# Kernel optimization log

Hardware: AMD Instinct MI355X
Metric: run time of the kernel (lower is better)

## Reference

```python
import jax, jax.numpy as jnp
import numpy as np

BS, RAL, LAL = 128, 1024, 256
CS, VOC, HFS, EMB = 256, 34, 512, 256


def setup_inputs() -> dict:
    key0 = jax.random.key(0)
    ks = jax.random.split(key0, 16)
    s = 0.02
    # mask from random valid lengths (at least 1 valid frame per example)
    lengths = jax.random.randint(ks[15], (BS,), RAL // 2, RAL + 1)
    mask = (jnp.arange(RAL)[None, :] < lengths[:, None]).astype(jnp.float32)
    return {
        "key": jax.random.normal(ks[0], (BS, RAL, CS), jnp.float32),
        "val": jax.random.normal(ks[1], (BS, RAL, CS), jnp.float32),
        "mask": mask,
        "emb": jax.random.normal(ks[2], (VOC, EMB), jnp.float32) * s,
        "Wih_a": jax.random.normal(ks[3], (4 * HFS, EMB + CS), jnp.float32) * s,
        "Whh_a": jax.random.normal(ks[4], (4 * HFS, HFS), jnp.float32) * s,
        "bih_a": jnp.zeros((4 * HFS,), jnp.float32),
        "bhh_a": jnp.zeros((4 * HFS,), jnp.float32),
        "Wih_b": jax.random.normal(ks[5], (4 * HFS, HFS), jnp.float32) * s,
        "Whh_b": jax.random.normal(ks[6], (4 * HFS, HFS), jnp.float32) * s,
        "bih_b": jnp.zeros((4 * HFS,), jnp.float32),
        "bhh_b": jnp.zeros((4 * HFS,), jnp.float32),
        "Wq": jax.random.normal(ks[7], (CS, HFS), jnp.float32) * s,
        "bq": jnp.zeros((CS,), jnp.float32),
        "Wc": jax.random.normal(ks[8], (VOC, HFS + CS), jnp.float32) * s,
        "bc": jnp.zeros((VOC,), jnp.float32),
        "y": jax.random.randint(ks[9], (BS, LAL), 0, VOC, jnp.int32),
    }


def _lstm_cell(x, h, c, Wih, Whh, bih, bhh):
    z = x @ Wih.T + bih + h @ Whh.T + bhh  # (BS, 4H)
    i, f, g, o = jnp.split(z, 4, axis=-1)
    i, f, o = jax.nn.sigmoid(i), jax.nn.sigmoid(f), jax.nn.sigmoid(o)
    g = jnp.tanh(g)
    c2 = f * c + i * g
    return o * jnp.tanh(c2), c2


def _attend(key, val, query, mask):
    # energy: (BS, RAL) = bmm(key, query[...,None])
    energy = jnp.einsum("brc,bc->br", key, query)
    att = jax.nn.softmax(energy, axis=1) * mask
    att = att / jnp.sum(att, axis=1, keepdims=True)
    return jnp.einsum("br,brc->bc", att, val)  # context (BS, CS)


def reference(key, val, mask, emb, Wih_a, Whh_a, bih_a, bhh_a,
              Wih_b, Whh_b, bih_b, bhh_b, Wq, bq, Wc, bc, y):
    bs = y.shape[0]
    z = jnp.zeros((bs, HFS), jnp.float32)
    init = (z, z, z, z, jnp.zeros((bs, CS), jnp.float32))

    def step(carry, y_t):
        ha, ca, hb, cb, ctx = carry
        e = emb[y_t]  # (BS, EMB)
        x = jnp.concatenate([e, ctx], axis=1)
        ha, ca = _lstm_cell(x, ha, ca, Wih_a, Whh_a, bih_a, bhh_a)
        hb, cb = _lstm_cell(ha, hb, cb, Wih_b, Whh_b, bih_b, bhh_b)
        query = hb @ Wq.T + bq  # (BS, CS)
        ctx = _attend(key, val, query, mask)
        logits = jnp.concatenate([hb, ctx], axis=1) @ Wc.T + bc  # (BS, VOC)
        return (ha, ca, hb, cb, ctx), logits

    _, preds = jax.lax.scan(step, init, y.T)  # (LAL, BS, VOC)
    return jnp.transpose(preds, (1, 0, 2))  # (BS, LAL, VOC)
```

## Files before the change

kernel.cpp:

```cpp
#include <hip/hip_runtime.h>
#include <cstdint>
#include <cstddef>

static constexpr int BS  = 128;
static constexpr int RAL = 1024;
static constexpr int LAL = 256;
static constexpr int CS  = 256;
static constexpr int VOC = 34;
static constexpr int HFS = 512;
static constexpr int EMB = 256;

typedef float  f32x4  __attribute__((ext_vector_type(4)));
typedef short  bf16x8 __attribute__((ext_vector_type(8)));

static __device__ __forceinline__ float bflo(unsigned int u) {
    return __builtin_bit_cast(float, u << 16);
}
static __device__ __forceinline__ float bfhi(unsigned int u) {
    return __builtin_bit_cast(float, u & 0xffff0000u);
}
static __device__ __forceinline__ unsigned short f2bf(float f) {
    unsigned int x = __builtin_bit_cast(unsigned int, f);
    x = (x + 0x7fffu + ((x >> 16) & 1u)) >> 16;
    return (unsigned short)x;
}
static __device__ __forceinline__ float sigf(float x)   { return 1.0f / (1.0f + __expf(-x)); }
static __device__ __forceinline__ float tanhf_(float x) { return 1.0f - 2.0f / (__expf(2.0f * x) + 1.0f); }

__global__ void cvt4_kernel(const float4* __restrict__ in, ushort4* __restrict__ out, int n4) {
    int i  = blockIdx.x * blockDim.x + threadIdx.x;
    int st = gridDim.x * blockDim.x;
    for (; i < n4; i += st) {
        float4 v = in[i];
        ushort4 o;
        o.x = f2bf(v.x); o.y = f2bf(v.y); o.z = f2bf(v.z); o.w = f2bf(v.w);
        out[i] = o;
    }
}

__global__ __launch_bounds__(256) void len_kernel(const float* __restrict__ mask, int* __restrict__ Llen) {
    __shared__ int red[256];
    const int b = blockIdx.x, tid = threadIdx.x;
    int c = 0;
    for (int r = tid; r < RAL; r += 256) c += (mask[b * RAL + r] != 0.0f) ? 1 : 0;
    red[tid] = c;
    __syncthreads();
    for (int s = 128; s > 0; s >>= 1) {
        if (tid < s) red[tid] += red[tid + s];
        __syncthreads();
    }
    if (tid == 0) Llen[b] = red[0];
}

__global__ __launch_bounds__(256) void lstm_kernel(
    const unsigned short* __restrict__ p0, int s0,
    const unsigned short* __restrict__ p1, int s1,
    const unsigned short* __restrict__ p2, int s2,
    const unsigned short* __restrict__ p3, int s3,
    const int* __restrict__ yidx, int t,
    const unsigned short* __restrict__ Wih, const unsigned short* __restrict__ Whh,
    const float* __restrict__ bih, const float* __restrict__ bhh,
    float* __restrict__ cst,
    unsigned short* __restrict__ hout)
{
    __shared__ __align__(16) float zp[3][4][64][4];

    const int tid  = threadIdx.x;
    const int lane = tid & 63;
    const int wv   = tid >> 6;
    const int quad = lane >> 4;
    const int l16  = lane & 15;
    const int j    = blockIdx.x * 16 + l16;
    const int mrow = blockIdx.y * 16 + l16;

    const unsigned short* pa;
    const unsigned short* wb;
    {
        const unsigned short* const ps[4] = {p0, p1, p2, p3};
        const int ss[4] = {s0, s1, s2, s3};
        long rbase;
        if (wv == 0 && yidx) rbase = (long)yidx[mrow * LAL + t] * ss[0];
        else                 rbase = (long)mrow * ss[wv];
        pa = ps[wv] + rbase + quad * 8;
        const unsigned short* Wp = (wv < 2) ? Wih : Whh;
        wb = Wp + (wv & 1) * 256 + quad * 8;
    }

    const unsigned short* wg[4];
#pragma unroll
    for (int g = 0; g < 4; ++g) wg[g] = wb + (long)(g * HFS + j) * HFS;

    f32x4 acc[4];
#pragma unroll
    for (int g = 0; g < 4; ++g) acc[g] = (f32x4)0.0f;

#pragma unroll
    for (int kc = 0; kc < 8; ++kc) {
        bf16x8 a  = *(const bf16x8*)(pa + kc * 32);
        bf16x8 b0 = *(const bf16x8*)(wg[0] + kc * 32);
        bf16x8 b1 = *(const bf16x8*)(wg[1] + kc * 32);
        bf16x8 b2 = *(const bf16x8*)(wg[2] + kc * 32);
        bf16x8 b3 = *(const bf16x8*)(wg[3] + kc * 32);
        acc[0] = __builtin_amdgcn_mfma_f32_16x16x32_bf16(a, b0, acc[0], 0, 0, 0);
        acc[1] = __builtin_amdgcn_mfma_f32_16x16x32_bf16(a, b1, acc[1], 0, 0, 0);
        acc[2] = __builtin_amdgcn_mfma_f32_16x16x32_bf16(a, b2, acc[2], 0, 0, 0);
        acc[3] = __builtin_amdgcn_mfma_f32_16x16x32_bf16(a, b3, acc[3], 0, 0, 0);
    }

    if (wv != 0) {
#pragma unroll
        for (int g = 0; g < 4; ++g)
            *(f32x4*)&zp[wv - 1][g][lane][0] = acc[g];
    }
    __syncthreads();
    if (wv == 0) {
#pragma unroll
        for (int g = 0; g < 4; ++g) {
            acc[g] += *(const f32x4*)&zp[0][g][lane][0];
            acc[g] += *(const f32x4*)&zp[1][g][lane][0];
            acc[g] += *(const f32x4*)&zp[2][g][lane][0];
        }
        const float bI = bih[j]           + bhh[j];
        const float bF = bih[HFS + j]     + bhh[HFS + j];
        const float bG = bih[2 * HFS + j] + bhh[2 * HFS + j];
        const float bO = bih[3 * HFS + j] + bhh[3 * HFS + j];
#pragma unroll
        for (int r = 0; r < 4; ++r) {
            int m   = blockIdx.y * 16 + quad * 4 + r;
            int idx = m * HFS + j;
            float iv = sigf(acc[0][r] + bI);
            float fv = sigf(acc[1][r] + bF);
            float gv = tanhf_(acc[2][r] + bG);
            float ov = sigf(acc[3][r] + bO);
            float cn = fv * cst[idx] + iv * gv;
            cst[idx] = cn;
            hout[idx] = f2bf(ov * tanhf_(cn));
        }
    }
}

template <bool KVBF>
__global__ __launch_bounds__(1024) void attn_kernel(
    const void* __restrict__ keyp, const void* __restrict__ valp,
    const int* __restrict__ Llen,
    const unsigned short* __restrict__ hbv,
    const unsigned short* __restrict__ Wqb,
    const float* __restrict__ bq,
    const float* __restrict__ Wc, const float* __restrict__ bc,
    unsigned short* __restrict__ ctxbf,
    float* __restrict__ outp, int t)
{
    __shared__ __align__(16) float xcat[HFS + CS];
    __shared__ __align__(16) float q_lds[CS];
    __shared__ __align__(16) float e_lds[RAL];
    __shared__ __align__(16) float ctxp[16][CS];
    __shared__ float red[32];

    const int tid = threadIdx.x;
    const int b   = blockIdx.x;
    const int L   = Llen[b];

    if (tid < HFS) xcat[tid] = bflo((unsigned int)hbv[b * HFS + tid]);
    __syncthreads();

    {
        const int c  = tid >> 2;
        const int jj = tid & 3;
        const unsigned short* wr = Wqb + (long)c * HFS + jj * 128;
        const float* xr = &xcat[jj * 128];
        float qa = 0.0f;
#pragma unroll
        for (int k = 0; k < 128; k += 8) {
            uint4 u = *(const uint4*)(wr + k);
            float4 h0 = *(const float4*)(xr + k);
            float4 h1 = *(const float4*)(xr + k + 4);
            qa += bflo(u.x) * h0.x + bfhi(u.x) * h0.y
                + bflo(u.y) * h0.z + bfhi(u.y) * h0.w
                + bflo(u.z) * h1.x + bfhi(u.z) * h1.y
                + bflo(u.w) * h1.z + bfhi(u.w) * h1.w;
        }
        qa += __shfl_xor(qa, 1);
        qa += __shfl_xor(qa, 2);
        if (jj == 0) q_lds[c] = qa + bq[c];
    }
    __syncthreads();

    {
        const int jj   = tid & 7;
        const int rloc = tid >> 3;
        for (int r0 = 0; r0 < L; r0 += 128) {
            const int r = r0 + rloc;
            float acc = 0.0f;
            if (r < L) {
                if (KVBF) {
                    const unsigned short* kp = (const unsigned short*)keyp + ((long)b * RAL + r) * CS + jj * 32;
#pragma unroll
                    for (int i = 0; i < 4; ++i) {
                        uint4 u = *(const uint4*)(kp + i * 8);
                        const float* qp = &q_lds[jj * 32 + i * 8];
                        float4 qa  = *(const float4*)qp;
                        float4 qb2 = *(const float4*)(qp + 4);
                        acc += bflo(u.x) * qa.x  + bfhi(u.x) * qa.y
                             + bflo(u.y) * qa.z  + bfhi(u.y) * qa.w
                             + bflo(u.z) * qb2.x + bfhi(u.z) * qb2.y
                             + bflo(u.w) * qb2.z + bfhi(u.w) * qb2.w;
                    }
                } else {
                    const float* kp = (const float*)keyp + ((long)b * RAL + r) * CS + jj * 32;
#pragma unroll
                    for (int i = 0; i < 8; ++i) {
                        float4 kv = *(const float4*)(kp + i * 4);
                        float4 qa = *(const float4*)&q_lds[jj * 32 + i * 4];
                        acc += kv.x * qa.x + kv.y * qa.y + kv.z * qa.z + kv.w * qa.w;
                    }
                }
            }
            acc += __shfl_xor(acc, 1);
            acc += __shfl_xor(acc, 2);
            acc += __shfl_xor(acc, 4);
            if (jj == 0 && r < L) e_lds[r] = acc;
        }
    }
    __syncthreads();

    float pm = (tid < L) ? e_lds[tid] : -1e30f;
#pragma unroll
    for (int s = 32; s > 0; s >>= 1) pm = fmaxf(pm, __shfl_xor(pm, s));
    if ((tid & 63) == 0) red[tid >> 6] = pm;
    __syncthreads();
    float M = red[0];
#pragma unroll
    for (int i = 1; i < 16; ++i) M = fmaxf(M, red[i]);

    float ps = 0.0f;
    if (tid < L) { float v = __expf(e_lds[tid] - M); e_lds[tid] = v; ps = v; }
#pragma unroll
    for (int s = 32; s > 0; s >>= 1) ps += __shfl_xor(ps, s);
    if ((tid & 63) == 0) red[16 + (tid >> 6)] = ps;
    __syncthreads();
    float S = 0.0f;
#pragma unroll
    for (int i = 0; i < 16; ++i) S += red[16 + i];
    const float invS = 1.0f / S;

    {
        const int wv = tid >> 6;
        const int c4 = (tid & 63) * 4;
        float a0 = 0.f, a1 = 0.f, a2 = 0.f, a3 = 0.f;
        if (KVBF) {
            const unsigned short* vb = (const unsigned short*)valp + (long)b * RAL * CS + c4;
            int r = wv;
            for (; r + 48 < L; r += 64) {
                uint2 u0 = *(const uint2*)(vb + (long)(r)      * CS);
                uint2 u1 = *(const uint2*)(vb + (long)(r + 16) * CS);
                uint2 u2 = *(const uint2*)(vb + (long)(r + 32) * CS);
                uint2 u3 = *(const uint2*)(vb + (long)(r + 48) * CS);
                float w0 = e_lds[r], w1 = e_lds[r + 16], w2 = e_lds[r + 32], w3 = e_lds[r + 48];
                a0 += w0 * bflo(u0.x) + w1 * bflo(u1.x) + w2 * bflo(u2.x) + w3 * bflo(u3.x);
                a1 += w0 * bfhi(u0.x) + w1 * bfhi(u1.x) + w2 * bfhi(u2.x) + w3 * bfhi(u3.x);
                a2 += w0 * bflo(u0.y) + w1 * bflo(u1.y) + w2 * bflo(u2.y) + w3 * bflo(u3.y);
                a3 += w0 * bfhi(u0.y) + w1 * bfhi(u1.y) + w2 * bfhi(u2.y) + w3 * bfhi(u3.y);
            }
            for (; r < L; r += 16) {
                uint2 u = *(const uint2*)(vb + (long)r * CS);
                float w = e_lds[r];
                a0 += w * bflo(u.x); a1 += w * bfhi(u.x);
                a2 += w * bflo(u.y); a3 += w * bfhi(u.y);
            }
        } else {
            const float* vb = (const float*)valp + (long)b * RAL * CS + c4;
            int r = wv;
            for (; r + 48 < L; r += 64) {
                float4 v0 = *(const float4*)(vb + (long)(r)      * CS);
                float4 v1 = *(const float4*)(vb + (long)(r + 16) * CS);
                float4 v2 = *(const float4*)(vb + (long)(r + 32) * CS);
                float4 v3 = *(const float4*)(vb + (long)(r + 48) * CS);
                float w0 = e_lds[r], w1 = e_lds[r + 16], w2 = e_lds[r + 32], w3 = e_lds[r + 48];
                a0 += w0 * v0.x + w1 * v1.x + w2 * v2.x + w3 * v3.x;
                a1 += w0 * v0.y + w1 * v1.y + w2 * v2.y + w3 * v3.y;
                a2 += w0 * v0.z + w1 * v1.z + w2 * v2.z + w3 * v3.z;
                a3 += w0 * v0.w + w1 * v1.w + w2 * v2.w + w3 * v3.w;
            }
            for (; r < L; r += 16) {
                float4 v = *(const float4*)(vb + (long)r * CS);
                float w = e_lds[r];
                a0 += w * v.x; a1 += w * v.y; a2 += w * v.z; a3 += w * v.w;
            }
        }
        float4 out4 = {a0, a1, a2, a3};
        *(float4*)&ctxp[tid >> 6][c4] = out4;
    }
    __syncthreads();

    if (tid < CS) {
        float cv = 0.0f;
#pragma unroll
        for (int w = 0; w < 16; ++w) cv += ctxp[w][tid];
        cv *= invS;
        xcat[HFS + tid] = cv;
        ctxbf[b * CS + tid] = f2bf(cv);
    }
    __syncthreads();

    if (tid < VOC * 8) {
        const int v   = tid >> 3;
        const int jj2 = tid & 7;
        const float* wr = Wc + (long)v * (HFS + CS) + jj2 * 96;
        const float* xr = &xcat[jj2 * 96];
        float part = 0.0f;
#pragma unroll
        for (int i = 0; i < 24; ++i) {
            float4 wv4 = *(const float4*)(wr + i * 4);
            float4 xv  = *(const float4*)(xr + i * 4);
            part += wv4.x * xv.x + wv4.y * xv.y + wv4.z * xv.z + wv4.w * xv.w;
        }
        part += __shfl_xor(part, 1);
        part += __shfl_xor(part, 2);
        part += __shfl_xor(part, 4);
        if (jj2 == 0)
            outp[((long)b * LAL + t) * VOC + v] = part + bc[v];
    }
}

extern "C" void kernel_launch(void* const* d_in, const int* in_sizes, int n_in,
                              void* d_out, int out_size, void* d_ws, size_t ws_size,
                              hipStream_t stream)
{
    (void)in_sizes; (void)n_in; (void)out_size;
    const float* keyf  = (const float*)d_in[0];
    const float* valf  = (const float*)d_in[1];
    const float* mask  = (const float*)d_in[2];
    const float* embf  = (const float*)d_in[3];
    const float* WihAf = (const float*)d_in[4];
    const float* WhhAf = (const float*)d_in[5];
    const float* bihA  = (const float*)d_in[6];
    const float* bhhA  = (const float*)d_in[7];
    const float* WihBf = (const float*)d_in[8];
    const float* WhhBf = (const float*)d_in[9];
    const float* bihB  = (const float*)d_in[10];
    const float* bhhB  = (const float*)d_in[11];
    const float* Wqf   = (const float*)d_in[12];
    const float* bq    = (const float*)d_in[13];
    const float* Wc    = (const float*)d_in[14];
    const float* bc    = (const float*)d_in[15];
    const int*   y     = (const int*)d_in[16];
    float* outp = (float*)d_out;

    size_t off = 0;
    auto take = [&](size_t bytes) -> void* {
        void* p = (char*)d_ws + off;
        off += (bytes + 255) & ~(size_t)255;
        return p;
    };

    unsigned short* ha    = (unsigned short*)take((size_t)2 * BS * HFS * 2);
    unsigned short* hbuf  = (unsigned short*)take((size_t)2 * BS * HFS * 2);
    float*          ca    = (float*)take((size_t)BS * HFS * 4);
    float*          cbuf  = (float*)take((size_t)BS * HFS * 4);
    unsigned short* ctxbf = (unsigned short*)take((size_t)BS * CS * 2);
    size_t stateBytes = off;

    int*            Llen  = (int*)take((size_t)BS * 4);
    unsigned short* embb  = (unsigned short*)take((size_t)VOC * EMB * 2);
    unsigned short* WihAb = (unsigned short*)take((size_t)4 * HFS * HFS * 2);
    unsigned short* WhhAb = (unsigned short*)take((size_t)4 * HFS * HFS * 2);
    unsigned short* WihBb = (unsigned short*)take((size_t)4 * HFS * HFS * 2);
    unsigned short* WhhBb = (unsigned short*)take((size_t)4 * HFS * HFS * 2);
    unsigned short* Wqb   = (unsigned short*)take((size_t)CS * HFS * 2);

    const size_t kvBytes = (size_t)BS * RAL * CS * 2;
    unsigned short* keyb = nullptr;
    unsigned short* valb = nullptr;
    bool kvbf = false;
    bool keyInVal = false;
    if (off + 2 * (kvBytes + 256) <= ws_size) {
        keyb = (unsigned short*)take(kvBytes);
        valb = (unsigned short*)take(kvBytes);
        kvbf = true;
    } else if (off + kvBytes + 256 <= ws_size) {
        valb = (unsigned short*)take(kvBytes);
        keyb = (unsigned short*)d_in[1];
        kvbf = true;
        keyInVal = true;
    }

    hipMemsetAsync(d_ws, 0, stateBytes, stream);
    len_kernel<<<dim3(BS), dim3(256), 0, stream>>>(mask, Llen);

    auto cvt = [&](const float* src, unsigned short* dst, long n) {
        int n4 = (int)(n / 4);
        int blocks = (n4 + 255) / 256;
        if (blocks > 8192) blocks = 8192;
        cvt4_kernel<<<dim3(blocks), dim3(256), 0, stream>>>((const float4*)src, (ushort4*)dst, n4);
    };
    cvt(embf,  embb,  (long)VOC * EMB);
    cvt(WihAf, WihAb, (long)4 * HFS * HFS);
    cvt(WhhAf, WhhAb, (long)4 * HFS * HFS);
    cvt(WihBf, WihBb, (long)4 * HFS * HFS);
    cvt(WhhBf, WhhBb, (long)4 * HFS * HFS);
    cvt(Wqf,   Wqb,   (long)CS * HFS);
    if (kvbf) {
        if (keyInVal) {
            cvt(valf, valb, (long)BS * RAL * CS);
            cvt(keyf, keyb, (long)BS * RAL * CS);
        } else {
            cvt(keyf, keyb, (long)BS * RAL * CS);
            cvt(valf, valb, (long)BS * RAL * CS);
        }
    }

    for (int t = 0; t < LAL; ++t) {
        unsigned short* haIn  = ha   + (t & 1) * (BS * HFS);
        unsigned short* haOut = ha   + ((t + 1) & 1) * (BS * HFS);
        unsigned short* hbIn  = hbuf + (t & 1) * (BS * HFS);
        unsigned short* hbOut = hbuf + ((t + 1) & 1) * (BS * HFS);

        lstm_kernel<<<dim3(32, 8), dim3(256), 0, stream>>>(
            embb, EMB, ctxbf, CS, haIn, HFS, haIn + 256, HFS,
            y, t, WihAb, WhhAb, bihA, bhhA, ca, haOut);

        lstm_kernel<<<dim3(32, 8), dim3(256), 0, stream>>>(
            haOut, HFS, haOut + 256, HFS, hbIn, HFS, hbIn + 256, HFS,
            nullptr, t, WihBb, WhhBb, bihB, bhhB, cbuf, hbOut);

        if (kvbf)
            attn_kernel<true><<<dim3(BS), dim3(1024), 0, stream>>>(
                keyb, valb, Llen, hbOut, Wqb, bq, Wc, bc, ctxbf, outp, t);
        else
            attn_kernel<false><<<dim3(BS), dim3(1024), 0, stream>>>(
                keyf, valf, Llen, hbOut, Wqb, bq, Wc, bc, ctxbf, outp, t);
    }
}
```

Measured before the change: 12.95 ms.

## Split attention over sequence halves with partial softmax and combine kernel

Splits the per-batch attention over the sequence axis into two blocks per batch row. Each block computes a local max, sum and unnormalized context, and a new combine kernel rescales and merges the partials and then computes the logits. This is meant to fill more compute units during the bandwidth-bound key/value pass. In exchange it adds one kernel launch per step, duplicates the query projection, and writes partial results to global memory.

```diff
diff --git a/kernel.cpp b/kernel.cpp
--- a/kernel.cpp
+++ b/kernel.cpp
@@ -9,6 +9,9 @@
 static constexpr int VOC = 34;
 static constexpr int HFS = 512;
 static constexpr int EMB = 256;
+
+static constexpr int NSPLIT = 2;
+static constexpr int RSPL   = RAL / NSPLIT;
 
 typedef float  f32x4  __attribute__((ext_vector_type(4)));
 typedef short  bf16x8 __attribute__((ext_vector_type(8)));
@@ -140,34 +143,43 @@
 }
 
 template <bool KVBF>
-__global__ __launch_bounds__(1024) void attn_kernel(
+__global__ __launch_bounds__(1024) void attn_part_kernel(
     const void* __restrict__ keyp, const void* __restrict__ valp,
     const int* __restrict__ Llen,
     const unsigned short* __restrict__ hbv,
     const unsigned short* __restrict__ Wqb,
     const float* __restrict__ bq,
-    const float* __restrict__ Wc, const float* __restrict__ bc,
-    unsigned short* __restrict__ ctxbf,
-    float* __restrict__ outp, int t)
+    float* __restrict__ attM, float* __restrict__ attS,
+    float* __restrict__ attC)
 {
-    __shared__ __align__(16) float xcat[HFS + CS];
+    __shared__ __align__(16) float hb_l[HFS];
     __shared__ __align__(16) float q_lds[CS];
-    __shared__ __align__(16) float e_lds[RAL];
+    __shared__ __align__(16) float e_lds[RSPL];
     __shared__ __align__(16) float ctxp[16][CS];
     __shared__ float red[32];
 
-    const int tid = threadIdx.x;
-    const int b   = blockIdx.x;
-    const int L   = Llen[b];
-
-    if (tid < HFS) xcat[tid] = bflo((unsigned int)hbv[b * HFS + tid]);
+    const int tid   = threadIdx.x;
+    const int b     = blockIdx.x;
+    const int sp    = blockIdx.y;
+    const int L     = Llen[b];
+    const int rbase = sp * RSPL;
+    int nv = L - rbase;
+    if (nv > RSPL) nv = RSPL;
+
+    if (nv <= 0) {
+        if (tid < CS) attC[((long)b * NSPLIT + sp) * CS + tid] = 0.0f;
+        if (tid == 0) { attM[b * NSPLIT + sp] = -1e30f; attS[b * NSPLIT + sp] = 0.0f; }
+        return;
+    }
+
+    if (tid < HFS) hb_l[tid] = bflo((unsigned int)hbv[b * HFS + tid]);
     __syncthreads();
 
     {
         const int c  = tid >> 2;
         const int jj = tid & 3;
         const unsigned short* wr = Wqb + (long)c * HFS + jj * 128;
-        const float* xr = &xcat[jj * 128];
+        const float* xr = &hb_l[jj * 128];
         float qa = 0.0f;
 #pragma unroll
         for (int k = 0; k < 128; k += 8) {
@@ -188,12 +200,13 @@
     {
         const int jj   = tid & 7;
         const int rloc = tid >> 3;
-        for (int r0 = 0; r0 < L; r0 += 128) {
+        for (int r0 = 0; r0 < nv; r0 += 128) {
             const int r = r0 + rloc;
             float acc = 0.0f;
-            if (r < L) {
+            if (r < nv) {
                 if (KVBF) {
-                    const unsigned short* kp = (const unsigned short*)keyp + ((long)b * RAL + r) * CS + jj * 32;
+                    const unsigned short* kp = (const unsigned short*)keyp
+                        + ((long)b * RAL + rbase + r) * CS + jj * 32;
 #pragma unroll
                     for (int i = 0; i < 4; ++i) {
                         uint4 u = *(const uint4*)(kp + i * 8);
@@ -206,7 +219,8 @@
                              + bflo(u.w) * qb2.z + bfhi(u.w) * qb2.w;
                     }
                 } else {
-                    const float* kp = (const float*)keyp + ((long)b * RAL + r) * CS + jj * 32;
+                    const float* kp = (const float*)keyp
+                        + ((long)b * RAL + rbase + r) * CS + jj * 32;
 #pragma unroll
                     for (int i = 0; i < 8; ++i) {
                         float4 kv = *(const float4*)(kp + i * 4);
@@ -218,12 +232,12 @@
             acc += __shfl_xor(acc, 1);
             acc += __shfl_xor(acc, 2);
             acc += __shfl_xor(acc, 4);
-            if (jj == 0 && r < L) e_lds[r] = acc;
-        }
-    }
-    __syncthreads();
-
-    float pm = (tid < L) ? e_lds[tid] : -1e30f;
+            if (jj == 0 && r < nv) e_lds[r] = acc;
+        }
+    }
+    __syncthreads();
+
+    float pm = (tid < nv) ? e_lds[tid] : -1e30f;
 #pragma unroll
     for (int s = 32; s > 0; s >>= 1) pm = fmaxf(pm, __shfl_xor(pm, s));
     if ((tid & 63) == 0) red[tid >> 6] = pm;
@@ -233,7 +247,7 @@
     for (int i = 1; i < 16; ++i) M = fmaxf(M, red[i]);
 
     float ps = 0.0f;
-    if (tid < L) { float v = __expf(e_lds[tid] - M); e_lds[tid] = v; ps = v; }
+    if (tid < nv) { float v = __expf(e_lds[tid] - M); e_lds[tid] = v; ps = v; }
 #pragma unroll
     for (int s = 32; s > 0; s >>= 1) ps += __shfl_xor(ps, s);
     if ((tid & 63) == 0) red[16 + (tid >> 6)] = ps;
@@ -241,16 +255,18 @@
     float S = 0.0f;
 #pragma unroll
     for (int i = 0; i < 16; ++i) S += red[16 + i];
-    const float invS = 1.0f / S;
+
+    if (tid == 0) { attM[b * NSPLIT + sp] = M; attS[b * NSPLIT + sp] = S; }
 
     {
         const int wv = tid >> 6;
         const int c4 = (tid & 63) * 4;
         float a0 = 0.f, a1 = 0.f, a2 = 0.f, a3 = 0.f;
         if (KVBF) {
-            const unsigned short* vb = (const unsigned short*)valp + (long)b * RAL * CS + c4;
+            const unsigned short* vb = (const unsigned short*)valp
+                + ((long)b * RAL + rbase) * CS + c4;
             int r = wv;
-            for (; r + 48 < L; r += 64) {
+            for (; r + 48 < nv; r += 64) {
                 uint2 u0 = *(const uint2*)(vb + (long)(r)      * CS);
                 uint2 u1 = *(const uint2*)(vb + (long)(r + 16) * CS);
                 uint2 u2 = *(const uint2*)(vb + (long)(r + 32) * CS);
@@ -261,16 +277,16 @@
                 a2 += w0 * bflo(u0.y) + w1 * bflo(u1.y) + w2 * bflo(u2.y) + w3 * bflo(u3.y);
                 a3 += w0 * bfhi(u0.y) + w1 * bfhi(u1.y) + w2 * bfhi(u2.y) + w3 * bfhi(u3.y);
             }
-            for (; r < L; r += 16) {
+            for (; r < nv; r += 16) {
                 uint2 u = *(const uint2*)(vb + (long)r * CS);
                 float w = e_lds[r];
                 a0 += w * bflo(u.x); a1 += w * bfhi(u.x);
                 a2 += w * bflo(u.y); a3 += w * bfhi(u.y);
             }
         } else {
-            const float* vb = (const float*)valp + (long)b * RAL * CS + c4;
+            const float* vb = (const float*)valp + ((long)b * RAL + rbase) * CS + c4;
             int r = wv;
-            for (; r + 48 < L; r += 64) {
+            for (; r + 48 < nv; r += 64) {
                 float4 v0 = *(const float4*)(vb + (long)(r)      * CS);
                 float4 v1 = *(const float4*)(vb + (long)(r + 16) * CS);
                 float4 v2 = *(const float4*)(vb + (long)(r + 32) * CS);
@@ -281,7 +297,7 @@
                 a2 += w0 * v0.z + w1 * v1.z + w2 * v2.z + w3 * v3.z;
                 a3 += w0 * v0.w + w1 * v1.w + w2 * v2.w + w3 * v3.w;
             }
-            for (; r < L; r += 16) {
+            for (; r < nv; r += 16) {
                 float4 v = *(const float4*)(vb + (long)r * CS);
                 float w = e_lds[r];
                 a0 += w * v.x; a1 += w * v.y; a2 += w * v.z; a3 += w * v.w;
@@ -296,7 +312,47 @@
         float cv = 0.0f;
 #pragma unroll
         for (int w = 0; w < 16; ++w) cv += ctxp[w][tid];
-        cv *= invS;
+        attC[((long)b * NSPLIT + sp) * CS + tid] = cv;
+    }
+}
+
+__global__ __launch_bounds__(512) void attn_comb_kernel(
+    const float* __restrict__ attM, const float* __restrict__ attS,
+    const float* __restrict__ attC,
+    const unsigned short* __restrict__ hbv,
+    const float* __restrict__ Wc, const float* __restrict__ bc,
+    unsigned short* __restrict__ ctxbf,
+    float* __restrict__ outp, int t)
+{
+    __shared__ __align__(16) float xcat[HFS + CS];
+    __shared__ float wsc[NSPLIT];
+
+    const int tid = threadIdx.x;
+    const int b   = blockIdx.x;
+
+    if (tid == 0) {
+        float M = attM[b * NSPLIT];
+#pragma unroll
+        for (int s = 1; s < NSPLIT; ++s) M = fmaxf(M, attM[b * NSPLIT + s]);
+        float S = 0.0f;
+        float w[NSPLIT];
+#pragma unroll
+        for (int s = 0; s < NSPLIT; ++s) {
+            w[s] = __expf(attM[b * NSPLIT + s] - M);
+            S += w[s] * attS[b * NSPLIT + s];
+        }
+        const float invS = 1.0f / S;
+#pragma unroll
+        for (int s = 0; s < NSPLIT; ++s) wsc[s] = w[s] * invS;
+    }
+    if (tid < HFS) xcat[tid] = bflo((unsigned int)hbv[b * HFS + tid]);
+    __syncthreads();
+
+    if (tid < CS) {
+        float cv = 0.0f;
+#pragma unroll
+        for (int s = 0; s < NSPLIT; ++s)
+            cv += wsc[s] * attC[((long)b * NSPLIT + s) * CS + tid];
         xcat[HFS + tid] = cv;
         ctxbf[b * CS + tid] = f2bf(cv);
     }
@@ -368,6 +424,10 @@
     unsigned short* WhhBb = (unsigned short*)take((size_t)4 * HFS * HFS * 2);
     unsigned short* Wqb   = (unsigned short*)take((size_t)CS * HFS * 2);
 
+    float* attM = (float*)take((size_t)BS * NSPLIT * 4);
+    float* attS = (float*)take((size_t)BS * NSPLIT * 4);
+    float* attC = (float*)take((size_t)BS * NSPLIT * CS * 4);
+
     const size_t kvBytes = (size_t)BS * RAL * CS * 2;
     unsigned short* keyb = nullptr;
     unsigned short* valb = nullptr;
@@ -424,10 +484,13 @@
             nullptr, t, WihBb, WhhBb, bihB, bhhB, cbuf, hbOut);
 
         if (kvbf)
-            attn_kernel<true><<<dim3(BS), dim3(1024), 0, stream>>>(
-                keyb, valb, Llen, hbOut, Wqb, bq, Wc, bc, ctxbf, outp, t);
+            attn_part_kernel<true><<<dim3(BS, NSPLIT), dim3(1024), 0, stream>>>(
+                keyb, valb, Llen, hbOut, Wqb, bq, attM, attS, attC);
         else
-            attn_kernel<false><<<dim3(BS), dim3(1024), 0, stream>>>(
-                keyf, valf, Llen, hbOut, Wqb, bq, Wc, bc, ctxbf, outp, t);
-    }
-}
+            attn_part_kernel<false><<<dim3(BS, NSPLIT), dim3(1024), 0, stream>>>(
+                keyf, valf, Llen, hbOut, Wqb, bq, attM, attS, attC);
+
+        attn_comb_kernel<<<dim3(BS), dim3(512), 0, stream>>>(
+            attM, attS, attC, hbOut, Wc, bc, ctxbf, outp, t);
+    }
+}
```

After: 12.77 ms. Within noise of the previous version (-1.4%).
